# Performance work log

Hardware: AMD Instinct MI355X
Metric: run time of the kernel (lower is better)

The kernel has to match this reference:

```python
import jax, jax.numpy as jnp
import numpy as np

N_VERTICES = 500_000
N_EDGES = 16_000_000


def setup_inputs() -> dict:
    key = jax.random.key(0)
    k1, k2, k3 = jax.random.split(key, 3)
    # positive features keep A_ii and the scatter-sum denominator away from zero
    vertex_attr = jax.random.uniform(k1, (N_VERTICES, 2), dtype=jnp.float32, minval=0.1, maxval=1.1)
    edge_attr = jax.random.uniform(k2, (N_EDGES, 3), dtype=jnp.float32, minval=0.1, maxval=1.1)
    edgeij_pair = jax.random.randint(k3, (2, N_EDGES), 0, N_VERTICES, dtype=jnp.int32)
    return {"vertex_attr": vertex_attr, "edge_attr": edge_attr, "edgeij_pair": edgeij_pair}


def reference(vertex_attr, edge_attr, edgeij_pair):
    src = edgeij_pair[0]  # i (row) in PyG MetaLayer convention
    n_vertices = vertex_attr.shape[0]

    A_ij = edge_attr[:, 0]
    S_ij = edge_attr[:, 1]
    v_ij = edge_attr[:, 2]
    # (Layer1_EdgeUpdate appends w_ij = C_j as a 4th edge column, but that
    #  column is never read downstream, so it is omitted here.)

    # Layer1 vertex update: gammabar_i = sum_k A_ik / sum_k A_ik*S_ik*v_ik
    numerator = jax.ops.segment_sum(A_ij, src, num_segments=n_vertices)
    denominator = jax.ops.segment_sum(A_ij * S_ij * v_ij, src, num_segments=n_vertices)
    gammabar = numerator / denominator  # [N]

    A_ii = vertex_attr[:, 0]
    C_i = vertex_attr[:, 1]
    alpha = gammabar / A_ii  # [N]

    # Layer2 edge update: w_ij = (1 - C_i) * (-A_ij * alpha_i), i = src
    w_ij = (1.0 - C_i[src]) * (-A_ij * alpha[src])  # [E]
    return w_ij
```

## Files before the change

kernel.cpp:

```cpp
#include <hip/hip_runtime.h>


#define BINS 256
#define VSHIFT 11
#define VPB 2048
#define NBLK 1024
#define BT 256
#define SBT 512
#define FBT 512
#define SUB 4096
#define SPLIT 8

#define SC_A 524288.0f
#define SC_D 4194304.0f

typedef unsigned int u32;
typedef unsigned short u16;
typedef unsigned char u8;
typedef unsigned long long u64;

static __device__ __forceinline__ u32 f2h(float x) {
    _Float16 h = (_Float16)x; u16 u; __builtin_memcpy(&u, &h, 2); return (u32)u;
}
static __device__ __forceinline__ float h2f(u32 u) {
    u16 v = (u16)u; _Float16 h; __builtin_memcpy(&h, &v, 2); return (float)h;
}


__global__ void hist_k(const int* __restrict__ src, int ne, int chunk,
                       u32* __restrict__ bh) {
    __shared__ u32 h[BINS];
    if (threadIdx.x < BINS) h[threadIdx.x] = 0;
    __syncthreads();
    int lo = blockIdx.x * chunk;
    int hi = min(ne, lo + chunk);
    int n = hi - lo;
    int ngroups = (n + 3) >> 2;
    for (int g = threadIdx.x; g < ngroups; g += SBT) {
        int i = lo + (g << 2);
        if (i + 3 < hi) {
            int4 s = *reinterpret_cast<const int4*>(src + i);
            atomicAdd(&h[((u32)s.x) >> VSHIFT], 1u);
            atomicAdd(&h[((u32)s.y) >> VSHIFT], 1u);
            atomicAdd(&h[((u32)s.z) >> VSHIFT], 1u);
            atomicAdd(&h[((u32)s.w) >> VSHIFT], 1u);
        } else {
            for (int j = i; j < hi; ++j)
                atomicAdd(&h[((u32)src[j]) >> VSHIFT], 1u);
        }
    }
    __syncthreads();
    if (threadIdx.x < BINS)
        bh[(size_t)blockIdx.x * BINS + threadIdx.x] = h[threadIdx.x];
}

__global__ void scan_col_k(u32* __restrict__ bh, u32* __restrict__ bin_total) {
    const int IT = NBLK / BT;
    int bin = blockIdx.x, t = threadIdx.x;
    u32 v[IT];
    u32 tsum = 0;
    #pragma unroll
    for (int k = 0; k < IT; ++k) {
        v[k] = bh[(size_t)(IT * t + k) * BINS + bin];
        tsum += v[k];
    }
    int lane = t & 63, wv = t >> 6;
    u32 inc = tsum;
    #pragma unroll
    for (int d = 1; d < 64; d <<= 1) {
        u32 y = __shfl_up(inc, d);
        if (lane >= d) inc += y;
    }
    __shared__ u32 wsum[BT / 64];
    if (lane == 63) wsum[wv] = inc;
    __syncthreads();
    u32 wbase = 0;
    for (int w = 0; w < wv; ++w) wbase += wsum[w];
    u32 run = wbase + inc - tsum;
    #pragma unroll
    for (int k = 0; k < IT; ++k) {
        u32 c = v[k];
        bh[(size_t)(IT * t + k) * BINS + bin] = run;
        run += c;
    }
    if (t == BT - 1) bin_total[bin] = run;
}

__global__ void scan_bins_k(const u32* __restrict__ bin_total,
                            u32* __restrict__ bin_base) {
    int t = threadIdx.x;
    u32 a0 = (t < BINS) ? bin_total[t] : 0;
    int lane = t & 63, wv = t >> 6;
    u32 inc = a0;
    #pragma unroll
    for (int d = 1; d < 64; d <<= 1) {
        u32 y = __shfl_up(inc, d);
        if (lane >= d) inc += y;
    }
    __shared__ u32 wsum[BT / 64];
    if (lane == 63) wsum[wv] = inc;
    __syncthreads();
    u32 wbase = 0;
    for (int w = 0; w < wv; ++w) wbase += wsum[w];
    if (t < BINS) bin_base[t] = wbase + inc - a0;
    if (t == BINS - 1) bin_base[BINS] = wbase + inc;
}

__global__ __launch_bounds__(SBT, 2)
void scatter_k(const float* __restrict__ eattr,
               const int* __restrict__ src,
               const u32* __restrict__ bh,
               const u32* __restrict__ bin_base,
               uint2* __restrict__ rec,
               u16* __restrict__ ah,
               int ne, int chunk) {
    __shared__ u32 cur[BINS];
    __shared__ u32 lbase[BINS];
    __shared__ u32 loff[BINS];
    __shared__ u32 wsum[SBT / 64];
    __shared__ uint2 stage[SUB];
    int t = threadIdx.x;
    int lane = t & 63, wid = t >> 6;
    if (t < BINS)
        cur[t] = bin_base[t] + bh[(size_t)blockIdx.x * BINS + t];
    int lo = blockIdx.x * chunk;
    int hi = min(ne, lo + chunk);
    for (int base = lo; base < hi; base += SUB) {
        int n = min(SUB, hi - base);
        if (t < BINS) lbase[t] = 0;
        __syncthreads();
        uint2 pay[8];
        u8 pb[8];
        #pragma unroll
        for (int half = 0; half < 2; ++half) {
            int g = t + half * SBT;
            int o = g << 2;
            int i = base + o;
            if (o + 3 < n) {
                int4 sv = *reinterpret_cast<const int4*>(src + i);
                const float4* ea = reinterpret_cast<const float4*>(eattr + 3ll * i);
                float4 w0 = ea[0], w1 = ea[1], w2 = ea[2];
                float A[4] = {w0.x, w0.w, w1.z, w2.y};
                float D[4] = {w0.x * w0.y * w0.z, w0.w * w1.x * w1.y,
                              w1.z * w1.w * w2.x, w2.y * w2.z * w2.w};
                int S[4] = {sv.x, sv.y, sv.z, sv.w};
                ushort4 hv;
                u16* hp = &hv.x;
                #pragma unroll
                for (int j = 0; j < 4; ++j) {
                    u32 s = (u32)S[j];
                    u32 ni = __float2uint_rn(A[j] * SC_A);
                    u32 di = __float2uint_rn(D[j] * SC_D);
                    u32 b = s >> VSHIFT;
                    pay[half * 4 + j] = make_uint2((b << 24) | di,
                                                   (ni << VSHIFT) | (s & (VPB - 1)));
                    pb[half * 4 + j] = (u8)b;
                    hp[j] = (u16)f2h(A[j]);
                    atomicAdd(&lbase[b], 1u);
                }
                *reinterpret_cast<ushort4*>(ah + i) = hv;
            } else {
                #pragma unroll
                for (int j = 0; j < 4; ++j) {
                    int o2 = o + j;
                    if (o2 < n) {
                        int i2 = base + o2;
                        u32 s = (u32)src[i2];
                        float a  = eattr[3ll * i2];
                        float s1 = eattr[3ll * i2 + 1];
                        float v1 = eattr[3ll * i2 + 2];
                        u32 ni = __float2uint_rn(a * SC_A);
                        u32 di = __float2uint_rn(a * s1 * v1 * SC_D);
                        u32 b = s >> VSHIFT;
                        pay[half * 4 + j] = make_uint2((b << 24) | di,
                                                       (ni << VSHIFT) | (s & (VPB - 1)));
                        pb[half * 4 + j] = (u8)b;
                        ah[i2] = (u16)f2h(a);
                        atomicAdd(&lbase[b], 1u);
                    }
                }
            }
        }
        __syncthreads();
        u32 a0 = (t < BINS) ? lbase[t] : 0;
        u32 inc = a0;
        #pragma unroll
        for (int d = 1; d < 64; d <<= 1) {
            u32 y = __shfl_up(inc, d);
            if (lane >= d) inc += y;
        }
        if (lane == 63) wsum[wid] = inc;
        __syncthreads();
        u32 wb = 0;
        for (int w = 0; w < wid; ++w) wb += wsum[w];
        u32 ex = wb + inc - a0;
        if (t < BINS) { lbase[t] = ex; loff[t] = ex; }
        __syncthreads();
        #pragma unroll
        for (int k = 0; k < 8; ++k) {
            int o = ((t + (k >> 2) * SBT) << 2) + (k & 3);
            if (o < n) {
                u8 b = pb[k];
                u32 p = atomicAdd(&loff[b], 1u);
                stage[p] = pay[k];
            }
        }
        __syncthreads();
        for (int p = t; p < n; p += SBT) {
            uint2 q = stage[p];
            u32 b = q.x >> 24;
            rec[cur[b] + (u32)p - lbase[b]] = make_uint2(q.x & 0x00FFFFFFu, q.y);
        }
        __syncthreads();
        if (t < BINS) cur[t] += loff[t] - lbase[t];
        __syncthreads();
    }
}

__global__ void accum_part_k(const uint2* __restrict__ rec,
                             const u32* __restrict__ bin_base,
                             u64* __restrict__ partial) {
    __shared__ u64 acc[VPB];
    int bin = blockIdx.x / SPLIT;
    int q   = blockIdx.x % SPLIT;
    for (int l = threadIdx.x; l < VPB; l += BT) acc[l] = 0ull;
    __syncthreads();
    u32 s0 = bin_base[bin], s1 = bin_base[bin + 1];
    u32 cnt = s1 - s0;
    u32 ra  = s0 + (u32)((u64)cnt * q / SPLIT);
    u32 rbn = s0 + (u32)((u64)cnt * (q + 1) / SPLIT);
    for (u32 r = ra + threadIdx.x; r < rbn; r += BT) {
        uint2 qq = rec[r];
        u64 add = ((u64)(qq.y >> VSHIFT) << 35) | (u64)qq.x;
        atomicAdd(&acc[qq.y & (VPB - 1)], add);
    }
    __syncthreads();
    u64* po = partial + (size_t)blockIdx.x * VPB;
    for (int l = threadIdx.x; l < VPB; l += BT) po[l] = acc[l];
}

__global__ void coef_part_k(const u64* __restrict__ partial,
                            const float* __restrict__ vattr,
                            float* __restrict__ coef, int nv) {
    int v = blockIdx.x * blockDim.x + threadIdx.x;
    int stride = gridDim.x * blockDim.x;
    for (; v < nv; v += stride) {
        int bin = v >> VSHIFT, l = v & (VPB - 1);
        size_t base = ((size_t)bin * SPLIT << VSHIFT) + l;
        float num = 0.f, den = 0.f;
        #pragma unroll
        for (int sp = 0; sp < SPLIT; ++sp) {
            u64 p = partial[base + ((size_t)sp << VSHIFT)];
            num += (float)(u32)(p >> 32);
            den += (float)(u32)p;
        }
        float2 va = reinterpret_cast<const float2*>(vattr)[v];
        float gam = num / den;
        coef[v] = (1.0f - va.y) * (-gam / va.x);
    }
}


#define FPSCALE 8388608.0f
#define FPINV   (1.0f / 8388608.0f)

__global__ void zero_u64(u64* __restrict__ p, int n) {
    int i = blockIdx.x * blockDim.x + threadIdx.x;
    int stride = gridDim.x * blockDim.x;
    for (; i < n; i += stride) p[i] = 0ull;
}

__global__ void accum_packed(const float* __restrict__ eattr,
                             const int* __restrict__ src,
                             u64* __restrict__ accp,
                             u16* __restrict__ ah, int ne) {
    int t = blockIdx.x * blockDim.x + threadIdx.x;
    int stride = gridDim.x * blockDim.x;
    for (int i = t; i < ne; i += stride) {
        float a = eattr[3ll * i];
        float d = a * eattr[3ll * i + 1] * eattr[3ll * i + 2];
        u32 ni = (u32)__float2uint_rn(a * FPSCALE);
        u32 di = (u32)__float2uint_rn(d * FPSCALE);
        atomicAdd(&accp[(u32)src[i]], ((u64)ni << 32) | (u64)di);
        if (ah) ah[i] = (u16)f2h(a);
    }
}

__global__ void coef_packed(const float* __restrict__ vattr,
                            const u64* __restrict__ accp,
                            float* __restrict__ coef, int nv) {
    int v = blockIdx.x * blockDim.x + threadIdx.x;
    int stride = gridDim.x * blockDim.x;
    for (; v < nv; v += stride) {
        u64 a = accp[v];
        float num = (float)(u32)(a >> 32) * FPINV;
        float den = (float)(u32)a * FPINV;
        float2 va = reinterpret_cast<const float2*>(vattr)[v];
        coef[v] = (1.0f - va.y) * (-(num / den) / va.x);
    }
}


__global__ void finalize(const u16* __restrict__ ah,
                         const float* __restrict__ edge_attr,
                         const int* __restrict__ src,
                         const float* __restrict__ coef,
                         float* __restrict__ out, int ne4, int n_edges) {
    int t = blockIdx.x * blockDim.x + threadIdx.x;
    int stride = gridDim.x * blockDim.x;
    for (int i = t; i < ne4; i += stride) {
        int4 s = reinterpret_cast<const int4*>(src)[i];
        float4 A;
        if (ah) {
            ushort4 h = reinterpret_cast<const ushort4*>(ah)[i];
            A.x = h2f(h.x); A.y = h2f(h.y); A.z = h2f(h.z); A.w = h2f(h.w);
        } else {
            const float* e = edge_attr + 12ll * i;
            A.x = e[0]; A.y = e[3]; A.z = e[6]; A.w = e[9];
        }
        float4 w;
        w.x = coef[s.x] * A.x;
        w.y = coef[s.y] * A.y;
        w.z = coef[s.z] * A.z;
        w.w = coef[s.w] * A.w;
        reinterpret_cast<float4*>(out)[i] = w;
    }
    for (int e = 4 * ne4 + t; e < n_edges; e += stride) {
        float Ae = ah ? h2f(ah[e]) : edge_attr[3ll * e];
        out[e] = coef[src[e]] * Ae;
    }
}

extern "C" void kernel_launch(void* const* d_in, const int* in_sizes, int n_in,
                              void* d_out, int out_size, void* d_ws, size_t ws_size,
                              hipStream_t stream) {
    const float* vattr = (const float*)d_in[0];
    const float* eattr = (const float*)d_in[1];
    const int*   pair  = (const int*)d_in[2];
    int nv = in_sizes[0] / 2;
    int ne = in_sizes[1] / 3;
    const int* src = pair;
    float* out = (float*)d_out;

    int ne4 = ne / 4;
    auto capped = [](long long want, int cap) {
        return (int)(want < cap ? (want > 1 ? want : 1) : cap);
    };
    int fgrid = capped(((long long)ne4 + FBT - 1) / FBT, 8192);

    size_t off = 0;
    float* coef = (float*)((char*)d_ws + off); off += (size_t)nv * 4;
    off = (off + 255) & ~(size_t)255;
    u32* bin_total = (u32*)((char*)d_ws + off); off += (size_t)BINS * 4;
    u32* bin_base  = (u32*)((char*)d_ws + off); off += (size_t)(BINS + 1) * 4;
    off = (off + 255) & ~(size_t)255;
    u32* bh  = (u32*)((char*)d_ws + off); off += (size_t)NBLK * BINS * 4;
    off = (off + 255) & ~(size_t)255;
    u64* partial = (u64*)((char*)d_ws + off); off += ((size_t)BINS * SPLIT << VSHIFT) * 8;
    off = (off + 255) & ~(size_t)255;
    uint2* rec = (uint2*)((char*)d_ws + off); off += 8ull * ne;
    off = (off + 255) & ~(size_t)255;
    u16* ah = (u16*)((char*)d_ws + off); off += 2ull * ne;
    long long chunk_ll = ((((long long)ne + NBLK - 1) / NBLK) + SUB - 1) / SUB * SUB;
    bool main_ok = ws_size >= off && nv <= (BINS << VSHIFT) &&
                   chunk_ll * NBLK < 2147000000ll;
    int chunk = (int)chunk_ll;

    if (main_ok) {
        hist_k<<<NBLK, SBT, 0, stream>>>(src, ne, chunk, bh);
        scan_col_k<<<BINS, BT, 0, stream>>>(bh, bin_total);
        scan_bins_k<<<1, BT, 0, stream>>>(bin_total, bin_base);
        scatter_k<<<NBLK, SBT, 0, stream>>>(eattr, src, bh, bin_base, rec, ah, ne, chunk);
        accum_part_k<<<BINS * SPLIT, BT, 0, stream>>>(rec, bin_base, partial);
        coef_part_k<<<capped(((long long)nv + BT - 1) / BT, 2048), BT, 0, stream>>>(partial, vattr, coef, nv);
        finalize<<<fgrid, FBT, 0, stream>>>(ah, eattr, src, coef, out, ne4, ne);
    } else {
        u64* accp = (u64*)d_ws;
        float* fcoef = (float*)(accp + nv);
        size_t fb_base = (size_t)nv * 12;
        fb_base = (fb_base + 255) & ~(size_t)255;
        u16* fah = nullptr;
        if (ws_size >= fb_base + 2ull * ne)
            fah = (u16*)((char*)d_ws + fb_base);
        int zgrid = capped(((long long)nv + BT - 1) / BT, 2048);
        int agrid = capped(((long long)ne + BT - 1) / BT, 4096);
        int cgrid = capped(((long long)nv + BT - 1) / BT, 2048);
        zero_u64<<<zgrid, BT, 0, stream>>>(accp, nv);
        accum_packed<<<agrid, BT, 0, stream>>>(eattr, src, accp, fah, ne);
        coef_packed<<<cgrid, BT, 0, stream>>>(vattr, accp, fcoef, nv);
        finalize<<<fgrid, FBT, 0, stream>>>(fah, eattr, src, fcoef, out, ne4, ne);
    }
}
```

Before: 244.6 us.

## Pad per-bin record runs to even length for 16-byte scatter and accumulate

Each sub-chunk's per-bin run in the record array is rounded up to an even count and filled with a dummy zero record when odd. This lets the scatter write and the accumulate kernel read records as uint4 pairs instead of uint2. The histogram now counts per sub-chunk with the same rounding so the global offsets stay consistent. The cost is a larger record buffer, extra padding traffic and extra dummy atomic adds of zero.

```diff
diff --git a/kernel.cpp b/kernel.cpp
--- a/kernel.cpp
+++ b/kernel.cpp
@@ -10,6 +10,7 @@
 #define FBT 512
 #define SUB 4096
 #define SPLIT 8
+#define STAGE_N (SUB + BINS)
 
 #define SC_A 524288.0f
 #define SC_D 4194304.0f
@@ -30,28 +31,34 @@
 __global__ void hist_k(const int* __restrict__ src, int ne, int chunk,
                        u32* __restrict__ bh) {
     __shared__ u32 h[BINS];
-    if (threadIdx.x < BINS) h[threadIdx.x] = 0;
-    __syncthreads();
+    __shared__ u32 hacc[BINS];
+    int t = threadIdx.x;
+    if (t < BINS) hacc[t] = 0;
     int lo = blockIdx.x * chunk;
     int hi = min(ne, lo + chunk);
-    int n = hi - lo;
-    int ngroups = (n + 3) >> 2;
-    for (int g = threadIdx.x; g < ngroups; g += SBT) {
-        int i = lo + (g << 2);
-        if (i + 3 < hi) {
-            int4 s = *reinterpret_cast<const int4*>(src + i);
-            atomicAdd(&h[((u32)s.x) >> VSHIFT], 1u);
-            atomicAdd(&h[((u32)s.y) >> VSHIFT], 1u);
-            atomicAdd(&h[((u32)s.z) >> VSHIFT], 1u);
-            atomicAdd(&h[((u32)s.w) >> VSHIFT], 1u);
-        } else {
-            for (int j = i; j < hi; ++j)
-                atomicAdd(&h[((u32)src[j]) >> VSHIFT], 1u);
-        }
-    }
-    __syncthreads();
-    if (threadIdx.x < BINS)
-        bh[(size_t)blockIdx.x * BINS + threadIdx.x] = h[threadIdx.x];
+    for (int base = lo; base < hi; base += SUB) {
+        int n = min(SUB, hi - base);
+        if (t < BINS) h[t] = 0;
+        __syncthreads();
+        int ng = (n + 3) >> 2;
+        for (int g = t; g < ng; g += SBT) {
+            int i = base + (g << 2);
+            if (i + 3 < base + n) {
+                int4 s = *reinterpret_cast<const int4*>(src + i);
+                atomicAdd(&h[((u32)s.x) >> VSHIFT], 1u);
+                atomicAdd(&h[((u32)s.y) >> VSHIFT], 1u);
+                atomicAdd(&h[((u32)s.z) >> VSHIFT], 1u);
+                atomicAdd(&h[((u32)s.w) >> VSHIFT], 1u);
+            } else {
+                for (int j = i; j < base + n; ++j)
+                    atomicAdd(&h[((u32)src[j]) >> VSHIFT], 1u);
+            }
+        }
+        __syncthreads();
+        if (t < BINS) hacc[t] += (h[t] + 1u) & ~1u;
+        __syncthreads();
+    }
+    if (t < BINS) bh[(size_t)blockIdx.x * BINS + t] = hacc[t];
 }
 
 __global__ void scan_col_k(u32* __restrict__ bh, u32* __restrict__ bin_total) {
@@ -118,7 +125,9 @@
     __shared__ u32 lbase[BINS];
     __shared__ u32 loff[BINS];
     __shared__ u32 wsum[SBT / 64];
-    __shared__ uint2 stage[SUB];
+    __shared__ u32 tot_s;
+    __shared__ uint4 stage4[STAGE_N / 2];
+    uint2* stage = reinterpret_cast<uint2*>(stage4);
     int t = threadIdx.x;
     int lane = t & 63, wid = t >> 6;
     if (t < BINS)
@@ -182,8 +191,9 @@
             }
         }
         __syncthreads();
-        u32 a0 = (t < BINS) ? lbase[t] : 0;
-        u32 inc = a0;
+        u32 araw = (t < BINS) ? lbase[t] : 0;
+        u32 r0 = (araw + 1u) & ~1u;
+        u32 inc = r0;
         #pragma unroll
         for (int d = 1; d < 64; d <<= 1) {
             u32 y = __shfl_up(inc, d);
@@ -193,8 +203,9 @@
         __syncthreads();
         u32 wb = 0;
         for (int w = 0; w < wid; ++w) wb += wsum[w];
-        u32 ex = wb + inc - a0;
+        u32 ex = wb + inc - r0;
         if (t < BINS) { lbase[t] = ex; loff[t] = ex; }
+        if (t == BINS - 1) tot_s = ex + r0;
         __syncthreads();
         #pragma unroll
         for (int k = 0; k < 8; ++k) {
@@ -206,13 +217,24 @@
             }
         }
         __syncthreads();
-        for (int p = t; p < n; p += SBT) {
-            uint2 q = stage[p];
+        if (t < BINS) {
+            u32 raw = loff[t] - lbase[t];
+            if (raw & 1u) stage[loff[t]] = make_uint2((u32)t << 24, 0u);
+        }
+        __syncthreads();
+        u32 tot2 = tot_s >> 1;
+        for (u32 p2 = t; p2 < tot2; p2 += SBT) {
+            uint4 q = stage4[p2];
             u32 b = q.x >> 24;
-            rec[cur[b] + (u32)p - lbase[b]] = make_uint2(q.x & 0x00FFFFFFu, q.y);
-        }
-        __syncthreads();
-        if (t < BINS) cur[t] += loff[t] - lbase[t];
+            u32 idx = cur[b] + (p2 << 1) - lbase[b];
+            *reinterpret_cast<uint4*>(&rec[idx]) =
+                make_uint4(q.x & 0x00FFFFFFu, q.y, q.z & 0x00FFFFFFu, q.w);
+        }
+        __syncthreads();
+        if (t < BINS) {
+            u32 raw = loff[t] - lbase[t];
+            cur[t] += (raw + 1u) & ~1u;
+        }
         __syncthreads();
     }
 }
@@ -227,12 +249,16 @@
     __syncthreads();
     u32 s0 = bin_base[bin], s1 = bin_base[bin + 1];
     u32 cnt = s1 - s0;
-    u32 ra  = s0 + (u32)((u64)cnt * q / SPLIT);
-    u32 rbn = s0 + (u32)((u64)cnt * (q + 1) / SPLIT);
-    for (u32 r = ra + threadIdx.x; r < rbn; r += BT) {
-        uint2 qq = rec[r];
-        u64 add = ((u64)(qq.y >> VSHIFT) << 35) | (u64)qq.x;
-        atomicAdd(&acc[qq.y & (VPB - 1)], add);
+    u32 ra  = (u32)(((u64)cnt * q / SPLIT) & ~1ull);
+    u32 rbn = (u32)(((u64)cnt * (q + 1) / SPLIT) & ~1ull);
+    if (q == SPLIT - 1) rbn = cnt;
+    const uint4* rp = reinterpret_cast<const uint4*>(rec + s0);
+    for (u32 r2 = (ra >> 1) + threadIdx.x; r2 < (rbn >> 1); r2 += BT) {
+        uint4 qq = rp[r2];
+        u64 add0 = ((u64)(qq.y >> VSHIFT) << 35) | (u64)qq.x;
+        atomicAdd(&acc[qq.y & (VPB - 1)], add0);
+        u64 add1 = ((u64)(qq.w >> VSHIFT) << 35) | (u64)qq.z;
+        atomicAdd(&acc[qq.w & (VPB - 1)], add1);
     }
     __syncthreads();
     u64* po = partial + (size_t)blockIdx.x * VPB;
@@ -348,6 +374,10 @@
     };
     int fgrid = capped(((long long)ne4 + FBT - 1) / FBT, 8192);
 
+    long long chunk_ll = ((((long long)ne + NBLK - 1) / NBLK) + SUB - 1) / SUB * SUB;
+    long long nsub_total = (chunk_ll / SUB) * (long long)NBLK;
+    long long rec_cap = (long long)ne + nsub_total * BINS;
+
     size_t off = 0;
     float* coef = (float*)((char*)d_ws + off); off += (size_t)nv * 4;
     off = (off + 255) & ~(size_t)255;
@@ -358,12 +388,11 @@
     off = (off + 255) & ~(size_t)255;
     u64* partial = (u64*)((char*)d_ws + off); off += ((size_t)BINS * SPLIT << VSHIFT) * 8;
     off = (off + 255) & ~(size_t)255;
-    uint2* rec = (uint2*)((char*)d_ws + off); off += 8ull * ne;
+    uint2* rec = (uint2*)((char*)d_ws + off); off += 8ull * rec_cap;
     off = (off + 255) & ~(size_t)255;
     u16* ah = (u16*)((char*)d_ws + off); off += 2ull * ne;
-    long long chunk_ll = ((((long long)ne + NBLK - 1) / NBLK) + SUB - 1) / SUB * SUB;
     bool main_ok = ws_size >= off && nv <= (BINS << VSHIFT) &&
-                   chunk_ll * NBLK < 2147000000ll;
+                   chunk_ll * NBLK < 2100000000ll && rec_cap < 2100000000ll;
     int chunk = (int)chunk_ll;
 
     if (main_ok) {
```

Result: no change. 241.8 us (-1.1%).
